# Kernel tuning notes

Hardware: AMD Instinct MI355X
Metric: run time of the kernel (lower is better)

The kernel has to match this reference:

```python
import jax, jax.numpy as jnp
import numpy as np

N_NODES = 100000
N_EDGES = 1600000
IN_DIM, HID, OUT_DIM = 64, 128, 9


def _lin_params(key, fan_in, fan_out, bias=True):
    k1, k2 = jax.random.split(key)
    bound = 1.0 / np.sqrt(fan_in)
    W = jax.random.uniform(k1, (fan_in, fan_out), jnp.float32, -bound, bound)
    if bias:
        b = jax.random.uniform(k2, (fan_out,), jnp.float32, -bound, bound)
        return W, b
    return W


def setup_inputs() -> dict:
    key = jax.random.key(0)
    ks = jax.random.split(key, 12)
    x = jax.random.normal(ks[0], (N_NODES, IN_DIM), jnp.float32)
    edge_index = jax.random.randint(ks[1], (2, N_EDGES), 0, N_NODES, jnp.int64 if jax.config.jax_enable_x64 else jnp.int32)
    Wl1, bl1 = _lin_params(ks[2], IN_DIM, HID)
    Wr1 = _lin_params(ks[3], IN_DIM, HID, bias=False)
    Wl2, bl2 = _lin_params(ks[4], HID, HID)
    Wr2 = _lin_params(ks[5], HID, HID, bias=False)
    Wl3, bl3 = _lin_params(ks[6], HID, 2 * HID)
    Wr3 = _lin_params(ks[7], HID, 2 * HID, bias=False)
    Wfc, bfc = _lin_params(ks[8], 2 * HID, OUT_DIM)
    return {"x": x, "edge_index": edge_index,
            "Wl1": Wl1, "bl1": bl1, "Wr1": Wr1,
            "Wl2": Wl2, "bl2": bl2, "Wr2": Wr2,
            "Wl3": Wl3, "bl3": bl3, "Wr3": Wr3,
            "Wfc": Wfc, "bfc": bfc}


def _sage_conv(x, src, dst, Wl, bl, Wr):
    # PyG SAGEConv (mean aggr): out = lin_l(mean_{j->i} x_j) + lin_r(x_i)
    n = x.shape[0]
    summed = jax.ops.segment_sum(x[src], dst, num_segments=n)         # [N, d]
    deg = jax.ops.segment_sum(jnp.ones((src.shape[0],), x.dtype), dst, num_segments=n)
    mean = summed / jnp.maximum(deg, 1.0)[:, None]
    return mean @ Wl + bl + x @ Wr


def reference(x, edge_index, Wl1, bl1, Wr1, Wl2, bl2, Wr2, Wl3, bl3, Wr3, Wfc, bfc):
    src, dst = edge_index[0], edge_index[1]
    h = jax.nn.relu(_sage_conv(x, src, dst, Wl1, bl1, Wr1))
    h = jax.nn.relu(_sage_conv(h, src, dst, Wl2, bl2, Wr2))
    h = jax.nn.relu(_sage_conv(h, src, dst, Wl3, bl3, Wr3))
    return h @ Wfc + bfc
```

## Files before the change

### kernel.cpp

```cpp
#include <hip/hip_runtime.h>
#include <cstddef>
#include <cstdint>


typedef unsigned int uint_t;
typedef unsigned short ushort_t;
typedef __attribute__((ext_vector_type(8))) short short8;
typedef __attribute__((ext_vector_type(4))) float f32x4;

#define N_IN 64
#define N_HID 128
#define N_OUT 9

__device__ __forceinline__ ushort_t f2bf(float f) {
    uint_t u = __float_as_uint(f);
    u += 0x7fffu + ((u >> 16) & 1u);
    return (ushort_t)(u >> 16);
}
__device__ __forceinline__ float bf2f(ushort_t h) {
    return __uint_as_float(((uint_t)h) << 16);
}
__device__ __forceinline__ void async_ld16(const void* g, void* l) {
    __builtin_amdgcn_global_load_lds((const __attribute__((address_space(1))) void*)g,
                                     (__attribute__((address_space(3))) void*)l, 16, 0, 0);
}

__global__ void rank_kernel(const int* __restrict__ dst, int* __restrict__ degi,
                            int* __restrict__ rank, int E) {
    int e = blockIdx.x * 256 + threadIdx.x;
    if (e < E) rank[e] = atomicAdd(&degi[dst[e]], 1);
}

__global__ __launch_bounds__(256) void block_sum_kernel(const int* __restrict__ degi,
                                                        int* __restrict__ partial, int M) {
    __shared__ int sm[256];
    int i = blockIdx.x * 256 + threadIdx.x;
    sm[threadIdx.x] = (i < M) ? degi[i] : 0;
    __syncthreads();
    for (int s = 128; s > 0; s >>= 1) {
        if (threadIdx.x < s) sm[threadIdx.x] += sm[threadIdx.x + s];
        __syncthreads();
    }
    if (threadIdx.x == 0) partial[blockIdx.x] = sm[0];
}

__global__ __launch_bounds__(512) void top_scan_par(int* __restrict__ partial, int nb) {
    __shared__ int sm[512];
    const int i = threadIdx.x;
    const int v = (i < nb) ? partial[i] : 0;
    sm[i] = v;
    __syncthreads();
    for (int off = 1; off < 512; off <<= 1) {
        int t = (i >= off) ? sm[i - off] : 0;
        __syncthreads();
        sm[i] += t;
        __syncthreads();
    }
    if (i < nb) partial[i] = sm[i] - v;
}

__global__ __launch_bounds__(256) void apply_scan_kernel(
    const int* __restrict__ degi, const int* __restrict__ partial,
    int* __restrict__ row_start, float* __restrict__ invdeg, int M)
{
    __shared__ int sm[256];
    int i = blockIdx.x * 256 + threadIdx.x;
    int d = (i < M) ? degi[i] : 0;
    sm[threadIdx.x] = d;
    __syncthreads();
    for (int off = 1; off < 256; off <<= 1) {
        int v = (threadIdx.x >= off) ? sm[threadIdx.x - off] : 0;
        __syncthreads();
        sm[threadIdx.x] += v;
        __syncthreads();
    }
    if (i < M) {
        row_start[i] = partial[blockIdx.x] + sm[threadIdx.x] - d;
        invdeg[i] = 1.0f / fmaxf((float)d, 1.0f);
    }
}

__global__ void fill_kernel(const int* __restrict__ src, const int* __restrict__ dst,
                            const int* __restrict__ row_start, const int* __restrict__ rank,
                            int* __restrict__ colA, int E) {
    int e = blockIdx.x * 256 + threadIdx.x;
    if (e < E) colA[row_start[dst[e]] + rank[e]] = src[e];
}

__global__ void split_x_kernel(const float* __restrict__ X, ushort_t* __restrict__ xh,
                               ushort_t* __restrict__ xl, ushort_t* __restrict__ xrow, int M) {
    int idx = blockIdx.x * 256 + threadIdx.x;
    if (idx >= M * 8) return;
    const int node = idx >> 3;
    const int ch = idx & 7;
    const float4 f0 = *(const float4*)(X + (size_t)node * 64 + ch * 8);
    const float4 f1 = *(const float4*)(X + (size_t)node * 64 + ch * 8 + 4);
    float e[8] = {f0.x, f0.y, f0.z, f0.w, f1.x, f1.y, f1.z, f1.w};
    uint_t hv[4], lv[4];
#pragma unroll
    for (int t = 0; t < 4; ++t) {
        ushort_t h0 = f2bf(e[2 * t]), h1 = f2bf(e[2 * t + 1]);
        ushort_t l0 = f2bf(e[2 * t] - bf2f(h0)), l1 = f2bf(e[2 * t + 1] - bf2f(h1));
        hv[t] = (uint_t)h0 | ((uint_t)h1 << 16);
        lv[t] = (uint_t)l0 | ((uint_t)l1 << 16);
    }
    const size_t off = ((size_t)(node >> 7) * 8 + ch) * 1024 + (node & 127) * 8;
    const uint4 hq = make_uint4(hv[0], hv[1], hv[2], hv[3]);
    *(uint4*)(xh + off) = hq;
    *(uint4*)(xl + off) = make_uint4(lv[0], lv[1], lv[2], lv[3]);
    *(uint4*)(xrow + (size_t)node * 64 + ch * 8) = hq;
}

__global__ __launch_bounds__(256) void wsplit_all(
    const float* __restrict__ Wl1, const float* __restrict__ Wr1,
    const float* __restrict__ Wl2, const float* __restrict__ Wr2,
    const float* __restrict__ Wl3, const float* __restrict__ Wr3,
    ushort_t* __restrict__ w1lh, ushort_t* __restrict__ w1ll,
    ushort_t* __restrict__ w1rh, ushort_t* __restrict__ w1rl,
    ushort_t* __restrict__ w2lh, ushort_t* __restrict__ w2ll,
    ushort_t* __restrict__ w2rh, ushort_t* __restrict__ w2rl,
    ushort_t* __restrict__ w3lh, ushort_t* __restrict__ w3ll,
    ushort_t* __restrict__ w3rh, ushort_t* __restrict__ w3rl)
{
    int idx = blockIdx.x * 256 + threadIdx.x;
    const float* W; ushort_t* th; ushort_t* tl; int K, N, e;
    if (idx < 8192)        { W = Wl1; th = w1lh; tl = w1ll; K = 64;  N = 128; e = idx; }
    else if (idx < 16384)  { W = Wr1; th = w1rh; tl = w1rl; K = 64;  N = 128; e = idx - 8192; }
    else if (idx < 32768)  { W = Wl2; th = w2lh; tl = w2ll; K = 128; N = 128; e = idx - 16384; }
    else if (idx < 49152)  { W = Wr2; th = w2rh; tl = w2rl; K = 128; N = 128; e = idx - 32768; }
    else if (idx < 81920)  { W = Wl3; th = w3lh; tl = w3ll; K = 128; N = 256; e = idx - 49152; }
    else if (idx < 114688) { W = Wr3; th = w3rh; tl = w3rl; K = 128; N = 256; e = idx - 81920; }
    else return;
    int k = e / N, n = e - k * N;
    float v = W[e];
    ushort_t hb = f2bf(v);
    const size_t off = ((size_t)(n >> 7) * (K >> 3) + (k >> 3)) * 1024 + (n & 127) * 8 + (k & 7);
    th[off] = hb;
    tl[off] = f2bf(v - bf2f(hb));
}

__device__ __forceinline__ void acc8_hi(float* a, uint4 h) {
    a[0] += __uint_as_float(h.x << 16);
    a[1] += __uint_as_float(h.x & 0xffff0000u);
    a[2] += __uint_as_float(h.y << 16);
    a[3] += __uint_as_float(h.y & 0xffff0000u);
    a[4] += __uint_as_float(h.z << 16);
    a[5] += __uint_as_float(h.z & 0xffff0000u);
    a[6] += __uint_as_float(h.w << 16);
    a[7] += __uint_as_float(h.w & 0xffff0000u);
}

template <int CH>
__global__ __launch_bounds__(256) void gather_mean_hi(
    const ushort_t* __restrict__ fh, const int* __restrict__ colA,
    const int* __restrict__ row_start, const int* __restrict__ degi,
    const float* __restrict__ invdeg,
    ushort_t* __restrict__ oh, int M)
{
    constexpr int SLOTS = 256 / CH;
    constexpr int DIM = CH * 8;
    const int tid = threadIdx.x;
    const int slot = tid / CH;
    const int ch = tid % CH;
    const int node = blockIdx.x * SLOTS + slot;
    if (node >= M) return;
    const int beg = row_start[node];
    const int cnt = degi[node];
    float a[8];
#pragma unroll
    for (int t = 0; t < 8; ++t) a[t] = 0.f;
    int j = 0;
    for (; j + 3 < cnt; j += 4) {
        const int s0 = colA[beg + j];
        const int s1 = colA[beg + j + 1];
        const int s2 = colA[beg + j + 2];
        const int s3 = colA[beg + j + 3];
        const uint4 h0 = *(const uint4*)(fh + (size_t)s0 * DIM + ch * 8);
        const uint4 h1 = *(const uint4*)(fh + (size_t)s1 * DIM + ch * 8);
        const uint4 h2 = *(const uint4*)(fh + (size_t)s2 * DIM + ch * 8);
        const uint4 h3 = *(const uint4*)(fh + (size_t)s3 * DIM + ch * 8);
        acc8_hi(a, h0);
        acc8_hi(a, h1);
        acc8_hi(a, h2);
        acc8_hi(a, h3);
    }
    for (; j < cnt; ++j) {
        const int s0 = colA[beg + j];
        const uint4 h0 = *(const uint4*)(fh + (size_t)s0 * DIM + ch * 8);
        acc8_hi(a, h0);
    }
    const float sc = invdeg[node];
    uint_t hv[4];
#pragma unroll
    for (int t = 0; t < 4; ++t) {
        ushort_t hb0 = f2bf(a[2 * t] * sc), hb1 = f2bf(a[2 * t + 1] * sc);
        hv[t] = (uint_t)hb0 | ((uint_t)hb1 << 16);
    }
    const size_t off = ((size_t)(node >> 7) * CH + ch) * 1024 + (node & 127) * 8;
    *(uint4*)(oh + off) = make_uint4(hv[0], hv[1], hv[2], hv[3]);
}

__global__ __launch_bounds__(256) void mfma_sage_gemm(
    const ushort_t* __restrict__ Amh,
    const ushort_t* __restrict__ Axh, const ushort_t* __restrict__ Axl,
    const ushort_t* __restrict__ Blh, const ushort_t* __restrict__ Bll,
    const ushort_t* __restrict__ Brh, const ushort_t* __restrict__ Brl,
    const float* __restrict__ bias, ushort_t* __restrict__ Oh,
    ushort_t* __restrict__ Orow,
    int M, int K, int N, int axl_valid)
{
    __shared__ ushort_t As_h[4096];
    __shared__ ushort_t As_l[4096];
    __shared__ ushort_t Bs_h[4096];
    __shared__ ushort_t Bs_l[4096];

    const int tid  = threadIdx.x;
    const int lane = tid & 63;
    const int wave = tid >> 6;
    const int wm = (wave & 1) * 64;
    const int wn = (wave >> 1) * 64;
    const int l15 = lane & 15;
    const int quad = lane >> 4;
    const int bm = blockIdx.x * 128;
    const int bn = blockIdx.y * 128;
    const int KC = K >> 3;

    const int s0 = wave * 1024 + lane * 8;
    const int s1 = s0 + 512;
    const size_t gA_w = ((size_t)blockIdx.x * KC + wave) << 10;
    const size_t gB_w = ((size_t)blockIdx.y * KC + wave) << 10;
    const int l8 = lane * 8;

    f32x4 acc[4][4];
#pragma unroll
    for (int i = 0; i < 4; ++i)
#pragma unroll
        for (int j = 0; j < 4; ++j) acc[i][j] = (f32x4){0.f, 0.f, 0.f, 0.f};

    for (int phase = 0; phase < 2; ++phase) {
        const ushort_t* __restrict__ Ah = phase ? Axh : Amh;
        const ushort_t* __restrict__ Al = phase ? Axl : (const ushort_t*)nullptr;
        const ushort_t* __restrict__ Bh = phase ? Brh : Blh;
        const ushort_t* __restrict__ Bl = phase ? Brl : Bll;
        const bool doAl = (phase == 1) && (axl_valid != 0);
        for (int k0 = 0; k0 < K; k0 += 32) {
            const size_t ga = gA_w + ((size_t)(k0 >> 3) << 10) + l8;
            const size_t gb = gB_w + ((size_t)(k0 >> 3) << 10) + l8;
            __syncthreads();
            async_ld16(Ah + ga, &As_h[s0]);
            async_ld16(Ah + ga + 512, &As_h[s1]);
            if (doAl) {
                async_ld16(Al + ga, &As_l[s0]);
                async_ld16(Al + ga + 512, &As_l[s1]);
            }
            async_ld16(Bh + gb, &Bs_h[s0]);
            async_ld16(Bh + gb + 512, &Bs_h[s1]);
            async_ld16(Bl + gb, &Bs_l[s0]);
            async_ld16(Bl + gb + 512, &Bs_l[s1]);
            __syncthreads();

            short8 fah[4], fal[4], fbh[4], fbl[4];
#pragma unroll
            for (int i = 0; i < 4; ++i) {
                const int aoff = quad * 1024 + (wm + i * 16 + l15) * 8;
                const int boff = quad * 1024 + (wn + i * 16 + l15) * 8;
                fah[i] = *(const short8*)&As_h[aoff];
                fbh[i] = *(const short8*)&Bs_h[boff];
                fbl[i] = *(const short8*)&Bs_l[boff];
                if (doAl) fal[i] = *(const short8*)&As_l[aoff];
            }
#pragma unroll
            for (int i = 0; i < 4; ++i)
#pragma unroll
                for (int j = 0; j < 4; ++j) {
                    acc[i][j] = __builtin_amdgcn_mfma_f32_16x16x32_bf16(fah[i], fbh[j], acc[i][j], 0, 0, 0);
                    acc[i][j] = __builtin_amdgcn_mfma_f32_16x16x32_bf16(fah[i], fbl[j], acc[i][j], 0, 0, 0);
                    if (doAl)
                        acc[i][j] = __builtin_amdgcn_mfma_f32_16x16x32_bf16(fal[i], fbh[j], acc[i][j], 0, 0, 0);
                }
        }
    }

    const size_t otile = (size_t)blockIdx.x * (N >> 3) * 1024;
#pragma unroll
    for (int i = 0; i < 4; ++i) {
        const int mr0 = wm + i * 16 + quad * 4;
#pragma unroll
        for (int j = 0; j < 4; ++j) {
            const int col = bn + wn + j * 16 + l15;
            const float bv = bias[col];
            const size_t cbase = otile + (size_t)(col >> 3) * 1024 + (col & 7);
#pragma unroll
            for (int r = 0; r < 4; ++r) {
                const int row = bm + mr0 + r;
                if (row < M) {
                    float y = fmaxf(acc[i][j][r] + bv, 0.f);
                    const ushort_t hb = f2bf(y);
                    Oh[cbase + (size_t)(mr0 + r) * 8] = hb;
                    if (Orow) Orow[(size_t)row * N + col] = hb;
                }
            }
        }
    }
}

__global__ __launch_bounds__(256) void fc_hi_kernel(
    const ushort_t* __restrict__ hh, const float* __restrict__ W,
    const float* __restrict__ b, float* __restrict__ outp, int M)
{
    __shared__ float Ws[256 * N_OUT];
    __shared__ float bs[N_OUT];
    for (int i = threadIdx.x; i < 256 * N_OUT; i += 256) Ws[i] = W[i];
    if (threadIdx.x < N_OUT) bs[threadIdx.x] = b[threadIdx.x];
    __syncthreads();
    const int t = blockIdx.x * 256 + threadIdx.x;
    if (t >= M * N_OUT) return;
    const int i = t / N_OUT;
    const int j = t - i * N_OUT;
    const ushort_t* __restrict__ base = hh + (size_t)(i >> 7) * 32 * 1024 + (i & 127) * 8;
    float s = bs[j];
#pragma unroll 4
    for (int c = 0; c < 32; ++c) {
        const uint4 v = *(const uint4*)(base + (size_t)c * 1024);
        const uint_t u[4] = {v.x, v.y, v.z, v.w};
#pragma unroll
        for (int q = 0; q < 4; ++q) {
            float a0 = __uint_as_float(u[q] << 16);
            float a1 = __uint_as_float(u[q] & 0xffff0000u);
            s += a0 * Ws[(c * 8 + 2 * q) * N_OUT + j] + a1 * Ws[(c * 8 + 2 * q + 1) * N_OUT + j];
        }
    }
    outp[t] = s;
}

extern "C" void kernel_launch(void* const* d_in, const int* in_sizes, int n_in,
                              void* d_out, int out_size, void* d_ws, size_t ws_size,
                              hipStream_t stream) {
    const float* x   = (const float*)d_in[0];
    const int*   ei  = (const int*)d_in[1];
    const float* Wl1 = (const float*)d_in[2];
    const float* bl1 = (const float*)d_in[3];
    const float* Wr1 = (const float*)d_in[4];
    const float* Wl2 = (const float*)d_in[5];
    const float* bl2 = (const float*)d_in[6];
    const float* Wr2 = (const float*)d_in[7];
    const float* Wl3 = (const float*)d_in[8];
    const float* bl3 = (const float*)d_in[9];
    const float* Wr3 = (const float*)d_in[10];
    const float* Wfc = (const float*)d_in[11];
    const float* bfc = (const float*)d_in[12];
    float* outp = (float*)d_out;

    const int M = in_sizes[0] / N_IN;
    const int E = in_sizes[1] / 2;
    const int* src = ei;
    const int* dst = ei + E;
    const int NB = (M + 255) / 256;
    const size_t Mrow = 100352;

    char* base = (char*)d_ws;
    char* p = base;
    int*   degi      = (int*)p;   p += Mrow * 4;
    int*   row_start = (int*)p;   p += Mrow * 4;
    int*   partial   = (int*)p;   p += 4096;
    float* invdeg    = (float*)p; p += Mrow * 4;
    int*   colA      = (int*)p;   p += ((size_t)E + 3) / 4 * 16;
    int*   rankb     = (int*)p;   p += ((size_t)E + 3) / 4 * 16;
    ushort_t* xh     = (ushort_t*)p; p += Mrow * 64 * 2;
    ushort_t* xl     = (ushort_t*)p; p += Mrow * 64 * 2;
    ushort_t* xrow   = (ushort_t*)p; p += Mrow * 64 * 2;
    ushort_t* h1h    = (ushort_t*)p; p += Mrow * 128 * 2;
    ushort_t* h1row  = (ushort_t*)p; p += Mrow * 128 * 2;
    size_t r0_used = (size_t)(p - base);
    size_t h3_need = Mrow * 256 * 2;
    ushort_t* h3h = (ushort_t*)base;
    p = base + (r0_used > h3_need ? r0_used : h3_need);
    ushort_t* aggh  = (ushort_t*)p; p += Mrow * 128 * 2;
    ushort_t* h2h   = (ushort_t*)p; p += Mrow * 128 * 2;
    ushort_t* h2row = (ushort_t*)p; p += Mrow * 128 * 2;
    ushort_t* w1lh = (ushort_t*)p; p += 64 * 128 * 2;
    ushort_t* w1ll = (ushort_t*)p; p += 64 * 128 * 2;
    ushort_t* w1rh = (ushort_t*)p; p += 64 * 128 * 2;
    ushort_t* w1rl = (ushort_t*)p; p += 64 * 128 * 2;
    ushort_t* w2lh = (ushort_t*)p; p += 128 * 128 * 2;
    ushort_t* w2ll = (ushort_t*)p; p += 128 * 128 * 2;
    ushort_t* w2rh = (ushort_t*)p; p += 128 * 128 * 2;
    ushort_t* w2rl = (ushort_t*)p; p += 128 * 128 * 2;
    ushort_t* w3lh = (ushort_t*)p; p += 128 * 256 * 2;
    ushort_t* w3ll = (ushort_t*)p; p += 128 * 256 * 2;
    ushort_t* w3rh = (ushort_t*)p; p += 128 * 256 * 2;
    ushort_t* w3rl = (ushort_t*)p; p += 128 * 256 * 2;
    (void)ws_size; (void)n_in; (void)out_size;

    const int blk = 256;
    const int grid_m = (M + 127) / 128;

    hipMemsetAsync(degi, 0, Mrow * 4, stream);
    rank_kernel<<<(E + blk - 1) / blk, blk, 0, stream>>>(dst, degi, rankb, E);
    block_sum_kernel<<<NB, blk, 0, stream>>>(degi, partial, M);
    top_scan_par<<<1, 512, 0, stream>>>(partial, NB);
    apply_scan_kernel<<<NB, blk, 0, stream>>>(degi, partial, row_start, invdeg, M);
    fill_kernel<<<(E + blk - 1) / blk, blk, 0, stream>>>(src, dst, row_start, rankb, colA, E);

    split_x_kernel<<<((M * 8) + blk - 1) / blk, blk, 0, stream>>>(x, xh, xl, xrow, M);
    wsplit_all<<<448, blk, 0, stream>>>(Wl1, Wr1, Wl2, Wr2, Wl3, Wr3,
        w1lh, w1ll, w1rh, w1rl, w2lh, w2ll, w2rh, w2rl, w3lh, w3ll, w3rh, w3rl);

    gather_mean_hi<8><<<(M + 31) / 32, blk, 0, stream>>>(
        xrow, colA, row_start, degi, invdeg, aggh, M);
    mfma_sage_gemm<<<dim3(grid_m, 1), blk, 0, stream>>>(
        aggh, xh, xl, w1lh, w1ll, w1rh, w1rl, bl1, h1h, h1row, M, 64, 128, 1);

    gather_mean_hi<16><<<(M + 15) / 16, blk, 0, stream>>>(
        h1row, colA, row_start, degi, invdeg, aggh, M);
    mfma_sage_gemm<<<dim3(grid_m, 1), blk, 0, stream>>>(
        aggh, h1h, (const ushort_t*)nullptr, w2lh, w2ll, w2rh, w2rl, bl2, h2h, h2row, M, 128, 128, 0);

    gather_mean_hi<16><<<(M + 15) / 16, blk, 0, stream>>>(
        h2row, colA, row_start, degi, invdeg, aggh, M);
    mfma_sage_gemm<<<dim3(grid_m, 2), blk, 0, stream>>>(
        aggh, h2h, (const ushort_t*)nullptr, w3lh, w3ll, w3rh, w3rl, bl3, h3h, (ushort_t*)nullptr, M, 128, 256, 0);

    fc_hi_kernel<<<(M * N_OUT + blk - 1) / blk, blk, 0, stream>>>(
        h3h, Wfc, bfc, outp, M);
}
```

Before: 501.1 us.

## Build CSR via two-level bucketed counting sort with LDS atomics

Replaces the global-atomic rank/scan/fill CSR construction with a two-pass bucket sort. Edges are first counted into 128-node buckets per chunk using shared-memory atomics, then column- and top-level scans give offsets, edges are scattered into bucket order, and each bucket is sorted locally into final CSR. This swaps contended global atomics and random scatter for LDS atomics and more localized writes. It adds extra kernel passes, an intermediate edge buffer, and assumes at most 800 buckets and src indices that fit in 25 bits.

Result: faster. 463.2 us (-7.5%).

```diff
diff --git a/kernel.cpp b/kernel.cpp
--- a/kernel.cpp
+++ b/kernel.cpp
@@ -11,6 +11,8 @@
 #define N_IN 64
 #define N_HID 128
 #define N_OUT 9
+#define EB 512
+#define NBUCK_MAX 800
 
 __device__ __forceinline__ ushort_t f2bf(float f) {
     uint_t u = __float_as_uint(f);
@@ -25,66 +27,117 @@
                                      (__attribute__((address_space(3))) void*)l, 16, 0, 0);
 }
 
-__global__ void rank_kernel(const int* __restrict__ dst, int* __restrict__ degi,
-                            int* __restrict__ rank, int E) {
-    int e = blockIdx.x * 256 + threadIdx.x;
-    if (e < E) rank[e] = atomicAdd(&degi[dst[e]], 1);
-}
-
-__global__ __launch_bounds__(256) void block_sum_kernel(const int* __restrict__ degi,
-                                                        int* __restrict__ partial, int M) {
-    __shared__ int sm[256];
-    int i = blockIdx.x * 256 + threadIdx.x;
-    sm[threadIdx.x] = (i < M) ? degi[i] : 0;
-    __syncthreads();
-    for (int s = 128; s > 0; s >>= 1) {
-        if (threadIdx.x < s) sm[threadIdx.x] += sm[threadIdx.x + s];
-        __syncthreads();
-    }
-    if (threadIdx.x == 0) partial[blockIdx.x] = sm[0];
-}
-
-__global__ __launch_bounds__(512) void top_scan_par(int* __restrict__ partial, int nb) {
-    __shared__ int sm[512];
+__global__ __launch_bounds__(256) void csr_count(const int* __restrict__ dst,
+                                                 uint_t* __restrict__ cnt,
+                                                 int E, int nbuck, int chunk) {
+    __shared__ uint_t c[NBUCK_MAX];
+    for (int i = threadIdx.x; i < nbuck; i += 256) c[i] = 0;
+    __syncthreads();
+    const int beg = blockIdx.x * chunk;
+    const int end = min(beg + chunk, E);
+    for (int i = beg + threadIdx.x; i < end; i += 256)
+        atomicAdd(&c[dst[i] >> 7], 1u);
+    __syncthreads();
+    for (int i = threadIdx.x; i < nbuck; i += 256)
+        cnt[(size_t)blockIdx.x * nbuck + i] = c[i];
+}
+
+__global__ __launch_bounds__(512) void csr_colscan(uint_t* __restrict__ cnt,
+                                                   uint_t* __restrict__ total, int nbuck) {
+    __shared__ uint_t sm[512];
+    const int b = blockIdx.x;
+    const uint_t v = cnt[(size_t)threadIdx.x * nbuck + b];
+    sm[threadIdx.x] = v;
+    __syncthreads();
+    for (int off = 1; off < 512; off <<= 1) {
+        uint_t t = (threadIdx.x >= off) ? sm[threadIdx.x - off] : 0;
+        __syncthreads();
+        sm[threadIdx.x] += t;
+        __syncthreads();
+    }
+    cnt[(size_t)threadIdx.x * nbuck + b] = sm[threadIdx.x] - v;
+    if (threadIdx.x == 511) total[b] = sm[511];
+}
+
+__global__ __launch_bounds__(1024) void top_scan_1024(const uint_t* __restrict__ total,
+                                                      uint_t* __restrict__ basev, int nb) {
+    __shared__ uint_t sm[1024];
     const int i = threadIdx.x;
-    const int v = (i < nb) ? partial[i] : 0;
+    const uint_t v = (i < nb) ? total[i] : 0;
     sm[i] = v;
     __syncthreads();
-    for (int off = 1; off < 512; off <<= 1) {
-        int t = (i >= off) ? sm[i - off] : 0;
+    for (int off = 1; off < 1024; off <<= 1) {
+        uint_t t = (i >= off) ? sm[i - off] : 0;
         __syncthreads();
         sm[i] += t;
         __syncthreads();
     }
-    if (i < nb) partial[i] = sm[i] - v;
-}
-
-__global__ __launch_bounds__(256) void apply_scan_kernel(
-    const int* __restrict__ degi, const int* __restrict__ partial,
-    int* __restrict__ row_start, float* __restrict__ invdeg, int M)
-{
-    __shared__ int sm[256];
-    int i = blockIdx.x * 256 + threadIdx.x;
-    int d = (i < M) ? degi[i] : 0;
-    sm[threadIdx.x] = d;
-    __syncthreads();
-    for (int off = 1; off < 256; off <<= 1) {
-        int v = (threadIdx.x >= off) ? sm[threadIdx.x - off] : 0;
-        __syncthreads();
-        sm[threadIdx.x] += v;
-        __syncthreads();
-    }
-    if (i < M) {
-        row_start[i] = partial[blockIdx.x] + sm[threadIdx.x] - d;
-        invdeg[i] = 1.0f / fmaxf((float)d, 1.0f);
-    }
-}
-
-__global__ void fill_kernel(const int* __restrict__ src, const int* __restrict__ dst,
-                            const int* __restrict__ row_start, const int* __restrict__ rank,
-                            int* __restrict__ colA, int E) {
-    int e = blockIdx.x * 256 + threadIdx.x;
-    if (e < E) colA[row_start[dst[e]] + rank[e]] = src[e];
+    if (i < nb) basev[i] = sm[i] - v;
+}
+
+__global__ __launch_bounds__(256) void csr_scatter(const int* __restrict__ src,
+                                                   const int* __restrict__ dst,
+                                                   const uint_t* __restrict__ cnt,
+                                                   const uint_t* __restrict__ basev,
+                                                   uint_t* __restrict__ ebuf,
+                                                   int E, int nbuck, int chunk) {
+    __shared__ uint_t cur[NBUCK_MAX];
+    for (int i = threadIdx.x; i < nbuck; i += 256)
+        cur[i] = basev[i] + cnt[(size_t)blockIdx.x * nbuck + i];
+    __syncthreads();
+    const int beg = blockIdx.x * chunk;
+    const int end = min(beg + chunk, E);
+    for (int i = beg + threadIdx.x; i < end; i += 256) {
+        const int d = dst[i];
+        const uint_t pos = atomicAdd(&cur[d >> 7], 1u);
+        ebuf[pos] = ((uint_t)src[i] << 7) | (uint_t)(d & 127);
+    }
+}
+
+__global__ __launch_bounds__(256) void csr_final(const uint_t* __restrict__ ebuf,
+                                                 const uint_t* __restrict__ basev,
+                                                 const uint_t* __restrict__ total,
+                                                 int* __restrict__ colA,
+                                                 int* __restrict__ row_start,
+                                                 int* __restrict__ degi,
+                                                 float* __restrict__ invdeg, int M) {
+    __shared__ uint_t c128[128];
+    __shared__ uint_t cur[128];
+    __shared__ uint_t sm[256];
+    const int b = blockIdx.x;
+    const int nbase = b << 7;
+    const uint_t e0 = basev[b];
+    const uint_t T = total[b];
+    if (threadIdx.x < 128) c128[threadIdx.x] = 0;
+    __syncthreads();
+    for (uint_t i = threadIdx.x; i < T; i += 256)
+        atomicAdd(&c128[ebuf[e0 + i] & 127], 1u);
+    __syncthreads();
+    const uint_t v = (threadIdx.x < 128) ? c128[threadIdx.x] : 0;
+    sm[threadIdx.x] = v;
+    __syncthreads();
+    for (int off = 1; off < 128; off <<= 1) {
+        uint_t t = (threadIdx.x >= off) ? sm[threadIdx.x - off] : 0;
+        __syncthreads();
+        sm[threadIdx.x] += t;
+        __syncthreads();
+    }
+    if (threadIdx.x < 128) {
+        const uint_t ex = sm[threadIdx.x] - v;
+        cur[threadIdx.x] = ex;
+        const int node = nbase + threadIdx.x;
+        if (node < M) {
+            degi[node] = (int)v;
+            invdeg[node] = 1.0f / fmaxf((float)v, 1.0f);
+            row_start[node] = (int)(e0 + ex);
+        }
+    }
+    __syncthreads();
+    for (uint_t i = threadIdx.x; i < T; i += 256) {
+        const uint_t p = ebuf[e0 + i];
+        const uint_t pos = atomicAdd(&cur[p & 127], 1u);
+        colA[e0 + pos] = (int)(p >> 7);
+    }
 }
 
 __global__ void split_x_kernel(const float* __restrict__ X, ushort_t* __restrict__ xh,
@@ -355,17 +408,20 @@
     const int E = in_sizes[1] / 2;
     const int* src = ei;
     const int* dst = ei + E;
-    const int NB = (M + 255) / 256;
     const size_t Mrow = 100352;
+    const int nbuck = (M + 127) / 128;
+    const int chunk = (E + EB - 1) / EB;
 
     char* base = (char*)d_ws;
     char* p = base;
     int*   degi      = (int*)p;   p += Mrow * 4;
     int*   row_start = (int*)p;   p += Mrow * 4;
-    int*   partial   = (int*)p;   p += 4096;
     float* invdeg    = (float*)p; p += Mrow * 4;
+    uint_t* cnt      = (uint_t*)p; p += (size_t)EB * NBUCK_MAX * 4;
+    uint_t* totalv   = (uint_t*)p; p += NBUCK_MAX * 4;
+    uint_t* basev    = (uint_t*)p; p += NBUCK_MAX * 4;
+    uint_t* ebuf     = (uint_t*)p; p += ((size_t)E + 3) / 4 * 16;
     int*   colA      = (int*)p;   p += ((size_t)E + 3) / 4 * 16;
-    int*   rankb     = (int*)p;   p += ((size_t)E + 3) / 4 * 16;
     ushort_t* xh     = (ushort_t*)p; p += Mrow * 64 * 2;
     ushort_t* xl     = (ushort_t*)p; p += Mrow * 64 * 2;
     ushort_t* xrow   = (ushort_t*)p; p += Mrow * 64 * 2;
@@ -395,12 +451,11 @@
     const int blk = 256;
     const int grid_m = (M + 127) / 128;
 
-    hipMemsetAsync(degi, 0, Mrow * 4, stream);
-    rank_kernel<<<(E + blk - 1) / blk, blk, 0, stream>>>(dst, degi, rankb, E);
-    block_sum_kernel<<<NB, blk, 0, stream>>>(degi, partial, M);
-    top_scan_par<<<1, 512, 0, stream>>>(partial, NB);
-    apply_scan_kernel<<<NB, blk, 0, stream>>>(degi, partial, row_start, invdeg, M);
-    fill_kernel<<<(E + blk - 1) / blk, blk, 0, stream>>>(src, dst, row_start, rankb, colA, E);
+    csr_count<<<EB, blk, 0, stream>>>(dst, cnt, E, nbuck, chunk);
+    csr_colscan<<<nbuck, 512, 0, stream>>>(cnt, totalv, nbuck);
+    top_scan_1024<<<1, 1024, 0, stream>>>(totalv, basev, nbuck);
+    csr_scatter<<<EB, blk, 0, stream>>>(src, dst, cnt, basev, ebuf, E, nbuck, chunk);
+    csr_final<<<nbuck, blk, 0, stream>>>(ebuf, basev, totalv, colA, row_start, degi, invdeg, M);
 
     split_x_kernel<<<((M * 8) + blk - 1) / blk, blk, 0, stream>>>(x, xh, xl, xrow, M);
     wsplit_all<<<448, blk, 0, stream>>>(Wl1, Wr1, Wl2, Wr2, Wl3, Wr3,
```
